# Kernel tuning notes

Measured on AMD Instinct MI355X. Metric: run time of the kernel, lower is better.

The kernel has to match this reference:

```python
import jax, jax.numpy as jnp
import numpy as np
from jax import lax

C = 128; G = 8; K = 3; P = K * K; GC = C // G
N, H, W = 4, 96, 96
EPS = 1e-5

def conv_bn_silu(x, w, gamma, beta, rmean, rvar, stride, pad):
    # Conv2d(bias=False) + BatchNorm2d(eval) + SiLU, NCHW
    y = lax.conv_general_dilated(x, w, (stride, stride), [(pad, pad), (pad, pad)],
                                 dimension_numbers=('NCHW', 'OIHW', 'NCHW'))
    s = gamma / jnp.sqrt(rvar + EPS)
    y = y * s[None, :, None, None] + (beta - rmean * s)[None, :, None, None]
    return y * jax.nn.sigmoid(y)

def dcnv3(x, dw_w, dw_b, ln_g, ln_b, off_w, off_b, m_w, m_b, ip_w, ip_b, op_w, op_b):
    # InternImage DCNv3, channels-last input (N,H,W,C), k=3 s=1 pad=1 dil=1 group=G, offset_scale=1
    n, h, w, c = x.shape
    xp = x @ ip_w.T + ip_b  # input_proj
    # offset/mask branch: depthwise 3x3 conv + LayerNorm + GELU on the ORIGINAL input
    dw = lax.conv_general_dilated(x, dw_w, (1, 1), [(1, 1), (1, 1)],
                                  dimension_numbers=('NHWC', 'HWIO', 'NHWC'),
                                  feature_group_count=c) + dw_b
    dw = (dw - dw.mean(-1, keepdims=True)) / jnp.sqrt(dw.var(-1, keepdims=True) + EPS) * ln_g + ln_b
    dw = jax.nn.gelu(dw)
    off = (dw @ off_w.T + off_b).reshape(n, h, w, G, P, 2)  # (..., (dx, dy))
    m = jax.nn.softmax((dw @ m_w.T + m_b).reshape(n, h, w, G, P), -1)
    pad = 1
    hp, wp = h + 2 * pad, w + 2 * pad
    xpad = jnp.pad(xp, ((0, 0), (pad, pad), (pad, pad), (0, 0))).reshape(n, hp, wp, G, GC)
    ky, kx = jnp.meshgrid(jnp.arange(-1, 2, dtype=x.dtype), jnp.arange(-1, 2, dtype=x.dtype), indexing='ij')
    # absolute sampling coords in padded image (grid_sample align_corners=False equivalent)
    py = (jnp.arange(h, dtype=x.dtype) + pad)[None, :, None, None, None] + ky.reshape(-1) + off[..., 1]
    px = (jnp.arange(w, dtype=x.dtype) + pad)[None, None, :, None, None] + kx.reshape(-1) + off[..., 0]
    yf = jnp.floor(py); xf = jnp.floor(px)
    wy = py - yf; wx = px - xf
    y0 = yf.astype(jnp.int32); x0 = xf.astype(jnp.int32)
    n_idx = jnp.arange(n)[:, None, None, None, None]
    g_idx = jnp.arange(G)[None, None, None, :, None]

    def gat(yi, xi):
        valid = ((yi >= 0) & (yi < hp) & (xi >= 0) & (xi < wp)).astype(x.dtype)
        v = xpad[n_idx, jnp.clip(yi, 0, hp - 1), jnp.clip(xi, 0, wp - 1), g_idx]  # (n,h,w,G,P,GC)
        return v * valid[..., None]

    v = (gat(y0, x0) * ((1 - wy) * (1 - wx))[..., None]
         + gat(y0, x0 + 1) * ((1 - wy) * wx)[..., None]
         + gat(y0 + 1, x0) * (wy * (1 - wx))[..., None]
         + gat(y0 + 1, x0 + 1) * (wy * wx)[..., None])
    out = jnp.einsum('nhwgpc,nhwgp->nhwgc', v, m).reshape(n, h, w, c)
    return out @ op_w.T + op_b  # output_proj

def _forward(x0, x1, x2, conv_w, conv_g, conv_b, conv_rm, conv_rv,
             conv1_w, conv1_g, conv1_b, conv1_rm, conv1_rv,
             conv2_w, conv2_g, conv2_b, conv2_rm, conv2_rv,
             dw_w, dw_b, ln_g, ln_b, off_w, off_b, m_w, m_b, ip_w, ip_b, op_w, op_b):
    n, _, h, w = x0.shape
    # x1: 256 ch > 128 -> self.conv (1x1); smaller spatial -> bilinear upsample to HW
    y1 = conv_bn_silu(x1, conv_w, conv_g, conv_b, conv_rm, conv_rv, 1, 0)
    feat_up1 = jax.image.resize(y1, (n, C, h, w), method='bilinear')
    # x2: 64 ch < 128 -> self.conv1 (1x1); larger spatial -> self.conv2 (3x3 s2) to HW
    y2 = conv_bn_silu(x2, conv1_w, conv1_g, conv1_b, conv1_rm, conv1_rv, 1, 0)
    feat_up2 = conv_bn_silu(y2, conv2_w, conv2_g, conv2_b, conv2_rm, conv2_rv, 2, 1)
    d1 = dcnv3(feat_up1.transpose(0, 2, 3, 1), dw_w, dw_b, ln_g, ln_b, off_w, off_b, m_w, m_b, ip_w, ip_b, op_w, op_b)
    d2 = dcnv3(feat_up2.transpose(0, 2, 3, 1), dw_w, dw_b, ln_g, ln_b, off_w, off_b, m_w, m_b, ip_w, ip_b, op_w, op_b)
    a1 = jax.nn.relu(d1).transpose(0, 3, 1, 2)
    a2 = jax.nn.relu(d2).transpose(0, 3, 1, 2)
    return jnp.concatenate([a1, x0, a2], axis=1)  # (N, 3C, H, W)

def setup_inputs():
    ks = jax.random.split(jax.random.key(0), 24)
    f = jnp.float32
    return {
        'x0': jax.random.normal(ks[0], (N, C, H, W), f),
        'x1': jax.random.normal(ks[1], (N, 2 * C, H // 2, W // 2), f),
        'x2': jax.random.normal(ks[2], (N, C // 2, 2 * H, 2 * W), f),
        'conv_w': jax.random.normal(ks[3], (C, 2 * C, 1, 1), f) * 0.05,
        'conv_g': jnp.ones((C,), f), 'conv_b': jnp.zeros((C,), f),
        'conv_rm': jax.random.normal(ks[4], (C,), f) * 0.1,
        'conv_rv': jax.random.uniform(ks[5], (C,), f) + 0.5,
        'conv1_w': jax.random.normal(ks[6], (C, C // 2, 1, 1), f) * 0.08,
        'conv1_g': jnp.ones((C,), f), 'conv1_b': jnp.zeros((C,), f),
        'conv1_rm': jax.random.normal(ks[7], (C,), f) * 0.1,
        'conv1_rv': jax.random.uniform(ks[8], (C,), f) + 0.5,
        'conv2_w': jax.random.normal(ks[9], (C, C, 3, 3), f) * 0.03,
        'conv2_g': jnp.ones((C,), f), 'conv2_b': jnp.zeros((C,), f),
        'conv2_rm': jax.random.normal(ks[10], (C,), f) * 0.1,
        'conv2_rv': jax.random.uniform(ks[11], (C,), f) + 0.5,
        'dw_w': jax.random.normal(ks[12], (3, 3, 1, C), f) * 0.1,
        'dw_b': jnp.zeros((C,), f),
        'ln_g': jnp.ones((C,), f), 'ln_b': jnp.zeros((C,), f),
        'off_w': jax.random.normal(ks[13], (G * P * 2, C), f) * 0.01,
        'off_b': jnp.zeros((G * P * 2,), f),
        'm_w': jax.random.normal(ks[14], (G * P, C), f) * 0.05,
        'm_b': jnp.zeros((G * P,), f),
        'ip_w': jax.random.normal(ks[15], (C, C), f) * 0.05,
        'ip_b': jnp.zeros((C,), f),
        'op_w': jax.random.normal(ks[16], (C, C), f) * 0.05,
        'op_b': jnp.zeros((C,), f),
    }

def reference(x0, x1, x2, conv_w, conv_g, conv_b, conv_rm, conv_rv,
              conv1_w, conv1_g, conv1_b, conv1_rm, conv1_rv,
              conv2_w, conv2_g, conv2_b, conv2_rm, conv2_rv,
              dw_w, dw_b, ln_g, ln_b, off_w, off_b, m_w, m_b, ip_w, ip_b, op_w, op_b):
    return _forward(x0, x1, x2, conv_w, conv_g, conv_b, conv_rm, conv_rv,
                    conv1_w, conv1_g, conv1_b, conv1_rm, conv1_rv,
                    conv2_w, conv2_g, conv2_b, conv2_rm, conv2_rv,
                    dw_w, dw_b, ln_g, ln_b, off_w, off_b, m_w, m_b, ip_w, ip_b, op_w, op_b)
```

## Files before the change

kernel.cpp:

```cpp
#include <hip/hip_runtime.h>
#include <cstdint>
#include <cstddef>

#define EPSV 1e-5f
#define NPIX 9216
#define LDA 136
#define LDK 72

typedef __bf16 bf16;
typedef _Float16 f16;
typedef __attribute__((ext_vector_type(8))) __bf16 bf16x8;
typedef __attribute__((ext_vector_type(4))) __bf16 bf16x4;
typedef __attribute__((ext_vector_type(2))) _Float16 f16x2;
typedef __attribute__((ext_vector_type(4))) float  f32x4;

__device__ __forceinline__ float silu_f(float v) { return v / (1.f + __expf(-v)); }

__global__ __launch_bounds__(256) void prep_kernel(
    const float* __restrict__ conv_w, const float* __restrict__ conv_g,
    const float* __restrict__ conv_b, const float* __restrict__ conv_rm, const float* __restrict__ conv_rv,
    const float* __restrict__ conv1_w, const float* __restrict__ conv1_g,
    const float* __restrict__ conv1_b, const float* __restrict__ conv1_rm, const float* __restrict__ conv1_rv,
    const float* __restrict__ conv2_w, const float* __restrict__ conv2_g,
    const float* __restrict__ conv2_bb, const float* __restrict__ conv2_rm, const float* __restrict__ conv2_rv,
    const float* __restrict__ ip_w, const float* __restrict__ op_w,
    const float* __restrict__ off_w, const float* __restrict__ m_w,
    const float* __restrict__ off_b, const float* __restrict__ m_b,
    float* __restrict__ WTSf, bf16* __restrict__ WTSb)
{
  int idx = blockIdx.x * 256 + threadIdx.x;
  if (idx < 608) {
    if (idx < 128) {
      int co = idx;
      float s = conv_g[co] * rsqrtf(conv_rv[co] + EPSV);
      WTSf[idx] = conv_b[co] - conv_rm[co] * s;
    } else if (idx < 256) {
      int co = idx - 128;
      float s = conv1_g[co] * rsqrtf(conv1_rv[co] + EPSV);
      WTSf[idx] = conv1_b[co] - conv1_rm[co] * s;
    } else if (idx < 384) {
      int co = idx - 256;
      float s = conv2_g[co] * rsqrtf(conv2_rv[co] + EPSV);
      WTSf[idx] = conv2_bb[co] - conv2_rm[co] * s;
    } else {
      int col = idx - 384;
      WTSf[idx] = (col < 144) ? off_b[col] : (col < 216 ? m_b[col - 144] : 0.f);
    }
  } else {
    int j = idx - 608;
    if (j < 32768) {
      int co = j >> 8, ci = j & 255;
      float s = conv_g[co] * rsqrtf(conv_rv[co] + EPSV);
      WTSb[j] = (bf16)(conv_w[co * 256 + ci] * s);
    } else if (j < 40960) {
      int r = j - 32768; int co = r >> 6, ci = r & 63;
      float s = conv1_g[co] * rsqrtf(conv1_rv[co] + EPSV);
      WTSb[j] = (bf16)(conv1_w[co * 64 + ci] * s);
    } else if (j < 188416) {
      int r = j - 40960; int kp = r >> 14; int rr = r & 16383;
      int co = rr >> 7, ci = rr & 127;
      float s = conv2_g[co] * rsqrtf(conv2_rv[co] + EPSV);
      WTSb[j] = (bf16)(conv2_w[(co * 128 + ci) * 9 + kp] * s);
    } else if (j < 204800) {
      int r = j - 188416; int co = r >> 7, ci = r & 127;
      WTSb[j] = (bf16)ip_w[co * 128 + ci];
    } else if (j < 233472) {
      int r = j - 204800; int co = r >> 7, ci = r & 127;
      float v = (co < 144) ? off_w[co * 128 + ci] : (co < 216 ? m_w[(co - 144) * 128 + ci] : 0.f);
      WTSb[j] = (bf16)v;
    } else if (j < 249856) {
      int r = j - 233472; int co = r >> 7, ci = r & 127;
      WTSb[j] = (bf16)op_w[co * 128 + ci];
    }
  }
}

__global__ __launch_bounds__(256) void c1x1_mfma_kernel(
    const float* __restrict__ x, const bf16* __restrict__ W,
    const float* __restrict__ bias, int K, int HW, bf16* __restrict__ outb)
{
  __shared__ bf16 As[64 * LDK];
  __shared__ bf16 Bs[128 * LDK];
  int m0 = blockIdx.x << 6;
  int t = threadIdx.x;
  int n = m0 / HW; int hw0 = m0 - n * HW;
  const float* xn = x + (size_t)n * K * HW;
  int wv = t >> 6, lane = t & 63;
  int lrow = lane & 15, q = lane >> 4;
  int n0 = wv * 32;
  f32x4 acc[4][2];
#pragma unroll
  for (int i = 0; i < 4; ++i)
#pragma unroll
    for (int j = 0; j < 2; ++j)
#pragma unroll
      for (int e = 0; e < 4; ++e) acc[i][j][e] = 0.f;

  for (int k0 = 0; k0 < K; k0 += 64) {
    if (k0) __syncthreads();
    for (int i = t; i < 1024; i += 256) {
      int px = i & 63; int ci4 = (i >> 6) << 2;
      bf16x4 p;
#pragma unroll
      for (int j = 0; j < 4; ++j)
        p[j] = (bf16)xn[(size_t)(k0 + ci4 + j) * HW + hw0 + px];
      *(bf16x4*)&As[px * LDK + ci4] = p;
    }
    for (int i = t; i < 1024; i += 256) {
      int co = i >> 3; int k8 = (i & 7) << 3;
      *(bf16x8*)&Bs[co * LDK + k8] = *(const bf16x8*)&W[(size_t)co * K + k0 + k8];
    }
    __syncthreads();
#pragma unroll
    for (int ks = 0; ks < 2; ++ks) {
      int ko = ks * 32 + q * 8;
      bf16x8 bfr0 = *(const bf16x8*)&Bs[(n0 + lrow) * LDK + ko];
      bf16x8 bfr1 = *(const bf16x8*)&Bs[(n0 + 16 + lrow) * LDK + ko];
#pragma unroll
      for (int mi = 0; mi < 4; ++mi) {
        bf16x8 afr = *(const bf16x8*)&As[(mi * 16 + lrow) * LDK + ko];
        acc[mi][0] = __builtin_amdgcn_mfma_f32_16x16x32_bf16(afr, bfr0, acc[mi][0], 0, 0, 0);
        acc[mi][1] = __builtin_amdgcn_mfma_f32_16x16x32_bf16(afr, bfr1, acc[mi][1], 0, 0, 0);
      }
    }
  }
#pragma unroll
  for (int mi = 0; mi < 4; ++mi) {
#pragma unroll
    for (int nj = 0; nj < 2; ++nj) {
      int co = n0 + nj * 16 + lrow;
      float bb = bias[co];
#pragma unroll
      for (int r = 0; r < 4; ++r) {
        int m = m0 + mi * 16 + q * 4 + r;
        outb[(size_t)m * 128 + co] = (bf16)silu_f(acc[mi][nj][r] + bb);
      }
    }
  }
}

__global__ __launch_bounds__(256) void upsample_kernel(
    const bf16* __restrict__ y1b, bf16* __restrict__ feat1b)
{
  int idx = blockIdx.x * 256 + threadIdx.x;
  int c4 = (idx & 31) << 2;
  int pw = idx >> 5;
  int ow = pw % 96; int t1 = pw / 96;
  int oh = t1 % 96; int n = t1 / 96;
  float sh = oh * 0.5f - 0.25f, sw = ow * 0.5f - 0.25f;
  float hf = floorf(sh), wf = floorf(sw);
  float fy = sh - hf, fx = sw - wf;
  int h0 = (int)hf, w0 = (int)wf;
  int h0c = max(h0, 0), h1c = min(h0 + 1, 47);
  int w0c = max(w0, 0), w1c = min(w0 + 1, 47);
  const bf16* yn = y1b + (size_t)n * 2304 * 128 + c4;
  bf16x4 v00 = *(const bf16x4*)&yn[(h0c * 48 + w0c) * 128];
  bf16x4 v01 = *(const bf16x4*)&yn[(h0c * 48 + w1c) * 128];
  bf16x4 v10 = *(const bf16x4*)&yn[(h1c * 48 + w0c) * 128];
  bf16x4 v11 = *(const bf16x4*)&yn[(h1c * 48 + w1c) * 128];
  bf16x4 o;
#pragma unroll
  for (int e = 0; e < 4; ++e) {
    float v = (1.f - fy) * ((1.f - fx) * (float)v00[e] + fx * (float)v01[e])
            + fy * ((1.f - fx) * (float)v10[e] + fx * (float)v11[e]);
    o[e] = (bf16)v;
  }
  *(bf16x4*)&feat1b[((size_t)n * NPIX + oh * 96 + ow) * 128 + c4] = o;
}

__global__ __launch_bounds__(256) void conv2_mfma_kernel(
    const bf16* __restrict__ y2b, const bf16* __restrict__ W2b,
    const float* __restrict__ b2, bf16* __restrict__ feat2b)
{
  __shared__ bf16 As[64 * LDA];
  __shared__ bf16 Bs[128 * LDA];
  int m0 = blockIdx.x << 6;
  int t = threadIdx.x;
  int wv = t >> 6, lane = t & 63;
  int lrow = lane & 15, q = lane >> 4;
  int n0 = wv * 32;
  f32x4 acc[4][2];
#pragma unroll
  for (int i = 0; i < 4; ++i)
#pragma unroll
    for (int j = 0; j < 2; ++j)
#pragma unroll
      for (int e = 0; e < 4; ++e) acc[i][j][e] = 0.f;
  bf16x8 zv;
#pragma unroll
  for (int e = 0; e < 8; ++e) zv[e] = (bf16)0.f;

  for (int kp = 0; kp < 9; ++kp) {
    int kh = kp / 3, kw = kp - kh * 3;
    __syncthreads();
    for (int i = t; i < 1024; i += 256) {
      int row = i >> 4; int c8 = (i & 15) << 3;
      int m = m0 + row;
      int nimg = m / NPIX; int hw = m - nimg * NPIX;
      int oh = hw / 96, ow = hw - oh * 96;
      int ih = 2 * oh - 1 + kh, iw = 2 * ow - 1 + kw;
      bf16x8 v = zv;
      if ((unsigned)ih < 192u && (unsigned)iw < 192u)
        v = *(const bf16x8*)&y2b[(((size_t)nimg * 192 + ih) * 192 + iw) * 128 + c8];
      *(bf16x8*)&As[row * LDA + c8] = v;
    }
    const bf16* Wk = W2b + kp * 16384;
    for (int i = t; i < 2048; i += 256) {
      int nn = i >> 4; int k8 = (i & 15) << 3;
      *(bf16x8*)&Bs[nn * LDA + k8] = *(const bf16x8*)&Wk[nn * 128 + k8];
    }
    __syncthreads();
#pragma unroll
    for (int ks = 0; ks < 4; ++ks) {
      bf16x8 bfr0 = *(const bf16x8*)&Bs[(n0 + lrow) * LDA + ks * 32 + q * 8];
      bf16x8 bfr1 = *(const bf16x8*)&Bs[(n0 + 16 + lrow) * LDA + ks * 32 + q * 8];
#pragma unroll
      for (int mi = 0; mi < 4; ++mi) {
        bf16x8 afr = *(const bf16x8*)&As[(mi * 16 + lrow) * LDA + ks * 32 + q * 8];
        acc[mi][0] = __builtin_amdgcn_mfma_f32_16x16x32_bf16(afr, bfr0, acc[mi][0], 0, 0, 0);
        acc[mi][1] = __builtin_amdgcn_mfma_f32_16x16x32_bf16(afr, bfr1, acc[mi][1], 0, 0, 0);
      }
    }
  }
#pragma unroll
  for (int mi = 0; mi < 4; ++mi) {
#pragma unroll
    for (int nj = 0; nj < 2; ++nj) {
      int co = n0 + nj * 16 + lrow;
      float bb = b2[co];
#pragma unroll
      for (int r = 0; r < 4; ++r) {
        int m = m0 + mi * 16 + q * 4 + r;
        feat2b[(size_t)m * 128 + co] = (bf16)silu_f(acc[mi][nj][r] + bb);
      }
    }
  }
}

__global__ __launch_bounds__(256) void mm_bf16_kernel(
    const bf16* __restrict__ A, const bf16* __restrict__ W,
    const float* __restrict__ bias, int Nc, int ostride, int act,
    int store_mode, void* __restrict__ outp)
{
  __shared__ bf16 As[64 * LDA];
  __shared__ bf16 Bs[128 * LDA];
  int m0 = blockIdx.x << 6;
  int nb = blockIdx.y << 7;
  int cols_here = Nc - nb; if (cols_here > 128) cols_here = 128;
  int t = threadIdx.x;
  for (int i = t; i < 1024; i += 256) {
    int row = i >> 4; int c8 = (i & 15) << 3;
    *(bf16x8*)&As[row * LDA + c8] = *(const bf16x8*)&A[(size_t)(m0 + row) * 128 + c8];
  }
  bf16x8 zv;
#pragma unroll
  for (int e = 0; e < 8; ++e) zv[e] = (bf16)0.f;
  for (int i = t; i < 2048; i += 256) {
    int n = i >> 4; int k8 = (i & 15) << 3;
    bf16x8 v = (n < cols_here) ? *(const bf16x8*)&W[(size_t)(nb + n) * 128 + k8] : zv;
    *(bf16x8*)&Bs[n * LDA + k8] = v;
  }
  __syncthreads();

  int wv = t >> 6, lane = t & 63;
  int lrow = lane & 15, q = lane >> 4;
  int n0 = wv * 32;
  f32x4 acc[4][2];
#pragma unroll
  for (int i = 0; i < 4; ++i)
#pragma unroll
    for (int j = 0; j < 2; ++j)
#pragma unroll
      for (int e = 0; e < 4; ++e) acc[i][j][e] = 0.f;

#pragma unroll
  for (int ks = 0; ks < 4; ++ks) {
    bf16x8 bfr0 = *(const bf16x8*)&Bs[(n0 + lrow) * LDA + ks * 32 + q * 8];
    bf16x8 bfr1 = *(const bf16x8*)&Bs[(n0 + 16 + lrow) * LDA + ks * 32 + q * 8];
#pragma unroll
    for (int mi = 0; mi < 4; ++mi) {
      bf16x8 afr = *(const bf16x8*)&As[(mi * 16 + lrow) * LDA + ks * 32 + q * 8];
      acc[mi][0] = __builtin_amdgcn_mfma_f32_16x16x32_bf16(afr, bfr0, acc[mi][0], 0, 0, 0);
      acc[mi][1] = __builtin_amdgcn_mfma_f32_16x16x32_bf16(afr, bfr1, acc[mi][1], 0, 0, 0);
    }
  }

  float* outf = (float*)outp;
  bf16*  outb = (bf16*)outp;
  f16*   outh = (f16*)outp;
#pragma unroll
  for (int mi = 0; mi < 4; ++mi) {
#pragma unroll
    for (int nj = 0; nj < 2; ++nj) {
      int col = nb + n0 + nj * 16 + lrow;
      if (col >= Nc) continue;
      float bb = bias[col];
#pragma unroll
      for (int r = 0; r < 4; ++r) {
        int m = m0 + mi * 16 + q * 4 + r;
        float v = acc[mi][nj][r] + bb;
        if (act == 1) v = fmaxf(v, 0.f);
        if (store_mode == 0) {
          outf[(size_t)m * ostride + col] = v;
        } else if (store_mode == 2) {
          outb[(size_t)m * 128 + col] = (bf16)v;
        } else if (store_mode == 3) {
          outh[(size_t)m * ostride + col] = (f16)v;
        } else {
          int nn = m / NPIX; int hw = m - nn * NPIX;
          int img = nn & 3; int choff = (nn >= 4) ? 256 : 0;
          outf[((size_t)(img * 384 + choff + col)) * NPIX + hw] = v;
        }
      }
    }
  }
}

__global__ __launch_bounds__(256) void dwln_kernel(
    const bf16* __restrict__ featb, const float* __restrict__ dw_w,
    const float* __restrict__ dw_b, const float* __restrict__ ln_g,
    const float* __restrict__ ln_b, bf16* __restrict__ dwgb)
{
  __shared__ float Wts[1152];
  __shared__ float Pb[384];
  int t = threadIdx.x;
  for (int i = t; i < 1152; i += 256) Wts[i] = dw_w[i];
  for (int i = t; i < 384; i += 256)
    Pb[i] = (i < 128) ? dw_b[i] : (i < 256 ? ln_g[i - 128] : ln_b[i - 256]);
  __syncthreads();

  int pxl = t >> 4;
  int c8 = (t & 15) << 3;
  int bid = blockIdx.x;
  int wg = (bid & 7) * 576 + (bid >> 3);
  int pixel = wg * 16 + pxl;
  int n = pixel / NPIX; int hw = pixel - n * NPIX;
  int h = hw / 96; int w = hw - h * 96;
  const bf16* fn = featb + (size_t)n * NPIX * 128 + c8;
  bf16x8 zv;
#pragma unroll
  for (int e = 0; e < 8; ++e) zv[e] = (bf16)0.f;

  bf16x8 v[9];
#pragma unroll
  for (int p = 0; p < 9; ++p) {
    int hh = h + p / 3 - 1, ww = w + (p % 3) - 1;
    bool valid = ((unsigned)hh < 96u) && ((unsigned)ww < 96u);
    int hc = min(max(hh, 0), 95), wc = min(max(ww, 0), 95);
    bf16x8 x = *(const bf16x8*)&fn[(hc * 96 + wc) * 128];
    v[p] = valid ? x : zv;
  }

  float acc[8];
#pragma unroll
  for (int e = 0; e < 8; ++e) acc[e] = Pb[c8 + e];
#pragma unroll
  for (int p = 0; p < 9; ++p) {
    f32x4 w0 = *(const f32x4*)&Wts[p * 128 + c8];
    f32x4 w1 = *(const f32x4*)&Wts[p * 128 + c8 + 4];
#pragma unroll
    for (int e = 0; e < 4; ++e) {
      acc[e]     += (float)v[p][e]     * w0[e];
      acc[4 + e] += (float)v[p][4 + e] * w1[e];
    }
  }

  float s = 0.f, qs = 0.f;
#pragma unroll
  for (int e = 0; e < 8; ++e) { s += acc[e]; qs += acc[e] * acc[e]; }
#pragma unroll
  for (int off = 8; off > 0; off >>= 1) {
    s  += __shfl_xor(s, off);
    qs += __shfl_xor(qs, off);
  }
  float mean = s * (1.f / 128.f);
  float var = qs * (1.f / 128.f) - mean * mean;
  float rstd = rsqrtf(var + EPSV);
  bf16x8 o;
#pragma unroll
  for (int e = 0; e < 8; ++e) {
    float xn = (acc[e] - mean) * rstd * Pb[128 + c8 + e] + Pb[256 + c8 + e];
    float z = 0.7978845608028654f * (xn + 0.044715f * xn * xn * xn);
    float th;
    if (z > 15.f) th = 1.f;
    else if (z < -15.f) th = -1.f;
    else { float e2 = __expf(2.f * z); th = (e2 - 1.f) / (e2 + 1.f); }
    o[e] = (bf16)(0.5f * xn * (1.f + th));
  }
  *(bf16x8*)&dwgb[(size_t)pixel * 128 + c8] = o;
}

__global__ __launch_bounds__(256, 6) void sample_kernel(
    const bf16* __restrict__ xpb, const f16* __restrict__ offm,
    const bf16* __restrict__ Wop, const float* __restrict__ op_b,
    float* __restrict__ out)
{
  __shared__ uint32_t Sd[16 * 112];
  __shared__ float Pm[16 * 72];
  __shared__ bf16 Avs[16 * LDA];
  const f16* S = (const f16*)Sd;
  int t = threadIdx.x;
  int bid = blockIdx.x;
  int wg = (bid & 7) * 576 + (bid >> 3);
  {
    const uint32_t* src = (const uint32_t*)(offm + (size_t)wg * 16 * 224);
    for (int i = t; i < 1792; i += 256) Sd[i] = src[i];
  }
  __syncthreads();
  if (t < 128) {
    int px = t >> 3, gg = t & 7;
    const f16* L = S + px * 224 + 144 + gg * 9;
    float l[9]; float mx = -1e30f;
#pragma unroll
    for (int p = 0; p < 9; ++p) { l[p] = (float)L[p]; mx = fmaxf(mx, l[p]); }
    float se = 0.f;
#pragma unroll
    for (int p = 0; p < 9; ++p) { l[p] = __expf(l[p] - mx); se += l[p]; }
    float inv = 1.f / se;
    float* Pp = Pm + px * 72 + gg * 9;
#pragma unroll
    for (int p = 0; p < 9; ++p) Pp[p] = l[p] * inv;
  }
  __syncthreads();
  int pxl = t >> 4;
  int tid16 = t & 15;
  int g = tid16 >> 1;
  int c8 = (tid16 & 1) << 3;
  int pixel = wg * 16 + pxl;
  int n = pixel / NPIX; int hw = pixel - n * NPIX;
  int h = hw / 96; int w = hw - h * 96;
  const f16* Sp = S + pxl * 224 + g * 18;
  const float* Pp = Pm + pxl * 72 + g * 9;
  const bf16* xpn = xpb + (size_t)n * NPIX * 128 + g * 16 + c8;
  float acc[8];
#pragma unroll
  for (int e = 0; e < 8; ++e) acc[e] = 0.f;
#pragma unroll 1
  for (int kh = 0; kh < 3; ++kh) {
#pragma unroll
    for (int kw = 0; kw < 3; ++kw) {
      int p = kh * 3 + kw;
      f16x2 d2 = *(const f16x2*)&Sp[p * 2];
      float dx = (float)d2.x, dy = (float)d2.y;
      float pyu = (float)(h + kh - 1) + dy;
      float pxu = (float)(w + kw - 1) + dx;
      float yf = floorf(pyu), xf = floorf(pxu);
      float wy = pyu - yf, wx = pxu - xf;
      int y0 = (int)yf, x0 = (int)xf;
      float ay0 = ((unsigned)y0 < 96u) ? (1.f - wy) : 0.f;
      float ay1 = ((unsigned)(y0 + 1) < 96u) ? wy : 0.f;
      float ax0 = ((unsigned)x0 < 96u) ? (1.f - wx) : 0.f;
      float ax1 = ((unsigned)(x0 + 1) < 96u) ? wx : 0.f;
      int y0c = min(max(y0, 0), 95), y1c = min(max(y0 + 1, 0), 95);
      int x0c = min(max(x0, 0), 95), x1c = min(max(x0 + 1, 0), 95);
      float mp = Pp[p];
      float w00 = ay0 * ax0 * mp, w01 = ay0 * ax1 * mp;
      float w10 = ay1 * ax0 * mp, w11 = ay1 * ax1 * mp;
      bf16x8 v00 = *(const bf16x8*)&xpn[(y0c * 96 + x0c) * 128];
      bf16x8 v01 = *(const bf16x8*)&xpn[(y0c * 96 + x1c) * 128];
      bf16x8 v10 = *(const bf16x8*)&xpn[(y1c * 96 + x0c) * 128];
      bf16x8 v11 = *(const bf16x8*)&xpn[(y1c * 96 + x1c) * 128];
#pragma unroll
      for (int e = 0; e < 8; ++e) {
        acc[e] += w00 * (float)v00[e] + w01 * (float)v01[e]
                + w10 * (float)v10[e] + w11 * (float)v11[e];
      }
    }
  }
  bf16x8 o;
#pragma unroll
  for (int e = 0; e < 8; ++e) o[e] = (bf16)acc[e];
  *(bf16x8*)&Avs[pxl * LDA + g * 16 + c8] = o;
  __syncthreads();

  {
    int wv = t >> 6, lane = t & 63;
    int lrow = lane & 15, q = lane >> 4;
    int n0 = wv * 32;
    f32x4 pacc[2];
#pragma unroll
    for (int j = 0; j < 2; ++j)
#pragma unroll
      for (int e = 0; e < 4; ++e) pacc[j][e] = 0.f;
#pragma unroll
    for (int ks = 0; ks < 4; ++ks) {
      int ko = ks * 32 + q * 8;
      bf16x8 afr  = *(const bf16x8*)&Avs[lrow * LDA + ko];
      bf16x8 bfr0 = *(const bf16x8*)&Wop[(size_t)(n0 + lrow) * 128 + ko];
      bf16x8 bfr1 = *(const bf16x8*)&Wop[(size_t)(n0 + 16 + lrow) * 128 + ko];
      pacc[0] = __builtin_amdgcn_mfma_f32_16x16x32_bf16(afr, bfr0, pacc[0], 0, 0, 0);
      pacc[1] = __builtin_amdgcn_mfma_f32_16x16x32_bf16(afr, bfr1, pacc[1], 0, 0, 0);
    }
    int nn = (wg * 16) / NPIX;
    int hwb = wg * 16 - nn * NPIX;
    int img = nn & 3; int choff = (nn >= 4) ? 256 : 0;
#pragma unroll
    for (int nj = 0; nj < 2; ++nj) {
      int col = n0 + nj * 16 + lrow;
      float bb = op_b[col];
      float* oc = out + ((size_t)(img * 384 + choff + col)) * NPIX + hwb;
#pragma unroll
      for (int r = 0; r < 4; ++r) {
        int px = q * 4 + r;
        oc[px] = fmaxf(pacc[nj][r] + bb, 0.f);
      }
    }
  }
}

__global__ __launch_bounds__(256) void copy_x0_kernel(
    const float4* __restrict__ x0, float4* __restrict__ out)
{
  int idx = blockIdx.x * 256 + threadIdx.x;
  int n = idx / (128 * 2304);
  int r = idx - n * (128 * 2304);
  out[(size_t)(n * 384 + 128) * 2304 + r] = x0[(size_t)n * 128 * 2304 + r];
}

extern "C" void kernel_launch(void* const* d_in, const int* in_sizes, int n_in,
                              void* d_out, int out_size, void* d_ws, size_t ws_size,
                              hipStream_t stream)
{
  (void)in_sizes; (void)n_in; (void)out_size; (void)ws_size;
  const float* x0      = (const float*)d_in[0];
  const float* x1      = (const float*)d_in[1];
  const float* x2      = (const float*)d_in[2];
  const float* conv_w  = (const float*)d_in[3];
  const float* conv_g  = (const float*)d_in[4];
  const float* conv_b  = (const float*)d_in[5];
  const float* conv_rm = (const float*)d_in[6];
  const float* conv_rv = (const float*)d_in[7];
  const float* conv1_w = (const float*)d_in[8];
  const float* conv1_g = (const float*)d_in[9];
  const float* conv1_b = (const float*)d_in[10];
  const float* conv1_rm= (const float*)d_in[11];
  const float* conv1_rv= (const float*)d_in[12];
  const float* conv2_w = (const float*)d_in[13];
  const float* conv2_g = (const float*)d_in[14];
  const float* conv2_b = (const float*)d_in[15];
  const float* conv2_rm= (const float*)d_in[16];
  const float* conv2_rv= (const float*)d_in[17];
  const float* dw_w    = (const float*)d_in[18];
  const float* dw_b    = (const float*)d_in[19];
  const float* ln_g    = (const float*)d_in[20];
  const float* ln_b    = (const float*)d_in[21];
  const float* off_w   = (const float*)d_in[22];
  const float* off_b   = (const float*)d_in[23];
  const float* m_w     = (const float*)d_in[24];
  const float* m_b     = (const float*)d_in[25];
  const float* ip_w    = (const float*)d_in[26];
  const float* ip_b    = (const float*)d_in[27];
  const float* op_w    = (const float*)d_in[28];
  const float* op_b    = (const float*)d_in[29];
  float* out = (float*)d_out;
  char* WS = (char*)d_ws;

  bf16* featb  = (bf16*)WS;
  bf16* feat1b = featb;
  bf16* feat2b = featb + 4718592;
  bf16* y2b    = (bf16*)(WS + 18874368);
  bf16* xpb    = (bf16*)(WS + 18874368);
  bf16* dwgb   = (bf16*)(WS + 37748736);
  bf16* y1b    = (bf16*)(WS + 56623104);
  f16*  offm   = (f16*)(WS + 58982400);
  float* WTSf  = (float*)(WS + 125042688);
  bf16*  WTSb  = (bf16*)(WS + 125045120);

  float* b1f  = WTSf;
  float* b1bf = WTSf + 128;
  float* b2f  = WTSf + 256;
  float* bomf = WTSf + 384;
  bf16* W1b  = WTSb;
  bf16* W1bb = WTSb + 32768;
  bf16* W2b  = WTSb + 40960;
  bf16* Wipb = WTSb + 188416;
  bf16* Womb = WTSb + 204800;
  bf16* Wopb = WTSb + 233472;

  prep_kernel<<<979, 256, 0, stream>>>(
      conv_w, conv_g, conv_b, conv_rm, conv_rv,
      conv1_w, conv1_g, conv1_b, conv1_rm, conv1_rv,
      conv2_w, conv2_g, conv2_b, conv2_rm, conv2_rv,
      ip_w, op_w, off_w, m_w, off_b, m_b, WTSf, WTSb);

  c1x1_mfma_kernel<<<144, 256, 0, stream>>>(x1, W1b, b1f, 256, 2304, y1b);
  upsample_kernel<<<4608, 256, 0, stream>>>(y1b, feat1b);

  c1x1_mfma_kernel<<<2304, 256, 0, stream>>>(x2, W1bb, b1bf, 64, 36864, y2b);
  conv2_mfma_kernel<<<576, 256, 0, stream>>>(y2b, W2b, b2f, feat2b);

  mm_bf16_kernel<<<dim3(1152, 1), 256, 0, stream>>>(featb, Wipb, ip_b, 128, 128, 0, 2, xpb);
  dwln_kernel<<<4608, 256, 0, stream>>>(featb, dw_w, dw_b, ln_g, ln_b, dwgb);
  mm_bf16_kernel<<<dim3(1152, 2), 256, 0, stream>>>(dwgb, Womb, bomf, 224, 224, 0, 3, offm);
  sample_kernel<<<4608, 256, 0, stream>>>(xpb, offm, Wopb, op_b, out);

  copy_x0_kernel<<<4608, 256, 0, stream>>>((const float4*)x0, (float4*)out);
}
```

Baseline: 384.0 us.

## Double sample-kernel pixel tile and stage output projection through LDS for coalesced stores

Each sample_kernel block now handles 32 pixels with 512 threads instead of 16 pixels with 256. The output-projection waves are split across row halves and column quarters. Results go into an LDS buffer that reuses the offset and mask storage, then are written to the NCHW output as float4 rows of 32 contiguous pixels per channel, replacing scattered 4-byte stores. The trade-offs are an extra barrier, more LDS per block, a launch bound of 6 blocks of 512 threads that may tighten register limits, and 16-byte LDS reads at a 33-float row stride whose alignment is not guaranteed.

```diff
diff --git a/kernel.cpp b/kernel.cpp
--- a/kernel.cpp
+++ b/kernel.cpp
@@ -390,24 +390,26 @@
   *(bf16x8*)&dwgb[(size_t)pixel * 128 + c8] = o;
 }
 
-__global__ __launch_bounds__(256, 6) void sample_kernel(
+__global__ __launch_bounds__(512, 6) void sample_kernel(
     const bf16* __restrict__ xpb, const f16* __restrict__ offm,
     const bf16* __restrict__ Wop, const float* __restrict__ op_b,
     float* __restrict__ out)
 {
-  __shared__ uint32_t Sd[16 * 112];
-  __shared__ float Pm[16 * 72];
-  __shared__ bf16 Avs[16 * LDA];
+  __shared__ char LB[32256];
+  uint32_t* Sd = (uint32_t*)LB;
+  float*    Pm = (float*)(LB + 14336);
+  bf16*     Avs = (bf16*)(LB + 23552);
+  float*    Cs = (float*)LB;
   const f16* S = (const f16*)Sd;
   int t = threadIdx.x;
   int bid = blockIdx.x;
-  int wg = (bid & 7) * 576 + (bid >> 3);
+  int wg = (bid & 7) * 288 + (bid >> 3);
   {
-    const uint32_t* src = (const uint32_t*)(offm + (size_t)wg * 16 * 224);
-    for (int i = t; i < 1792; i += 256) Sd[i] = src[i];
+    const uint32_t* src = (const uint32_t*)(offm + (size_t)wg * 32 * 224);
+    for (int i = t; i < 3584; i += 512) Sd[i] = src[i];
   }
   __syncthreads();
-  if (t < 128) {
+  if (t < 256) {
     int px = t >> 3, gg = t & 7;
     const f16* L = S + px * 224 + 144 + gg * 9;
     float l[9]; float mx = -1e30f;
@@ -422,61 +424,64 @@
     for (int p = 0; p < 9; ++p) Pp[p] = l[p] * inv;
   }
   __syncthreads();
-  int pxl = t >> 4;
-  int tid16 = t & 15;
-  int g = tid16 >> 1;
-  int c8 = (tid16 & 1) << 3;
-  int pixel = wg * 16 + pxl;
-  int n = pixel / NPIX; int hw = pixel - n * NPIX;
-  int h = hw / 96; int w = hw - h * 96;
-  const f16* Sp = S + pxl * 224 + g * 18;
-  const float* Pp = Pm + pxl * 72 + g * 9;
-  const bf16* xpn = xpb + (size_t)n * NPIX * 128 + g * 16 + c8;
-  float acc[8];
-#pragma unroll
-  for (int e = 0; e < 8; ++e) acc[e] = 0.f;
+  {
+    int pxl = t >> 4;
+    int tid16 = t & 15;
+    int g = tid16 >> 1;
+    int c8 = (tid16 & 1) << 3;
+    int pixel = wg * 32 + pxl;
+    int n = pixel / NPIX; int hw = pixel - n * NPIX;
+    int h = hw / 96; int w = hw - h * 96;
+    const f16* Sp = S + pxl * 224 + g * 18;
+    const float* Pp = Pm + pxl * 72 + g * 9;
+    const bf16* xpn = xpb + (size_t)n * NPIX * 128 + g * 16 + c8;
+    float acc[8];
+#pragma unroll
+    for (int e = 0; e < 8; ++e) acc[e] = 0.f;
 #pragma unroll 1
-  for (int kh = 0; kh < 3; ++kh) {
-#pragma unroll
-    for (int kw = 0; kw < 3; ++kw) {
-      int p = kh * 3 + kw;
-      f16x2 d2 = *(const f16x2*)&Sp[p * 2];
-      float dx = (float)d2.x, dy = (float)d2.y;
-      float pyu = (float)(h + kh - 1) + dy;
-      float pxu = (float)(w + kw - 1) + dx;
-      float yf = floorf(pyu), xf = floorf(pxu);
-      float wy = pyu - yf, wx = pxu - xf;
-      int y0 = (int)yf, x0 = (int)xf;
-      float ay0 = ((unsigned)y0 < 96u) ? (1.f - wy) : 0.f;
-      float ay1 = ((unsigned)(y0 + 1) < 96u) ? wy : 0.f;
-      float ax0 = ((unsigned)x0 < 96u) ? (1.f - wx) : 0.f;
-      float ax1 = ((unsigned)(x0 + 1) < 96u) ? wx : 0.f;
-      int y0c = min(max(y0, 0), 95), y1c = min(max(y0 + 1, 0), 95);
-      int x0c = min(max(x0, 0), 95), x1c = min(max(x0 + 1, 0), 95);
-      float mp = Pp[p];
-      float w00 = ay0 * ax0 * mp, w01 = ay0 * ax1 * mp;
-      float w10 = ay1 * ax0 * mp, w11 = ay1 * ax1 * mp;
-      bf16x8 v00 = *(const bf16x8*)&xpn[(y0c * 96 + x0c) * 128];
-      bf16x8 v01 = *(const bf16x8*)&xpn[(y0c * 96 + x1c) * 128];
-      bf16x8 v10 = *(const bf16x8*)&xpn[(y1c * 96 + x0c) * 128];
-      bf16x8 v11 = *(const bf16x8*)&xpn[(y1c * 96 + x1c) * 128];
-#pragma unroll
-      for (int e = 0; e < 8; ++e) {
-        acc[e] += w00 * (float)v00[e] + w01 * (float)v01[e]
-                + w10 * (float)v10[e] + w11 * (float)v11[e];
+    for (int kh = 0; kh < 3; ++kh) {
+#pragma unroll
+      for (int kw = 0; kw < 3; ++kw) {
+        int p = kh * 3 + kw;
+        f16x2 d2 = *(const f16x2*)&Sp[p * 2];
+        float dx = (float)d2.x, dy = (float)d2.y;
+        float pyu = (float)(h + kh - 1) + dy;
+        float pxu = (float)(w + kw - 1) + dx;
+        float yf = floorf(pyu), xf = floorf(pxu);
+        float wy = pyu - yf, wx = pxu - xf;
+        int y0 = (int)yf, x0 = (int)xf;
+        float ay0 = ((unsigned)y0 < 96u) ? (1.f - wy) : 0.f;
+        float ay1 = ((unsigned)(y0 + 1) < 96u) ? wy : 0.f;
+        float ax0 = ((unsigned)x0 < 96u) ? (1.f - wx) : 0.f;
+        float ax1 = ((unsigned)(x0 + 1) < 96u) ? wx : 0.f;
+        int y0c = min(max(y0, 0), 95), y1c = min(max(y0 + 1, 0), 95);
+        int x0c = min(max(x0, 0), 95), x1c = min(max(x0 + 1, 0), 95);
+        float mp = Pp[p];
+        float w00 = ay0 * ax0 * mp, w01 = ay0 * ax1 * mp;
+        float w10 = ay1 * ax0 * mp, w11 = ay1 * ax1 * mp;
+        bf16x8 v00 = *(const bf16x8*)&xpn[(y0c * 96 + x0c) * 128];
+        bf16x8 v01 = *(const bf16x8*)&xpn[(y0c * 96 + x1c) * 128];
+        bf16x8 v10 = *(const bf16x8*)&xpn[(y1c * 96 + x0c) * 128];
+        bf16x8 v11 = *(const bf16x8*)&xpn[(y1c * 96 + x1c) * 128];
+#pragma unroll
+        for (int e = 0; e < 8; ++e) {
+          acc[e] += w00 * (float)v00[e] + w01 * (float)v01[e]
+                  + w10 * (float)v10[e] + w11 * (float)v11[e];
+        }
       }
     }
-  }
-  bf16x8 o;
-#pragma unroll
-  for (int e = 0; e < 8; ++e) o[e] = (bf16)acc[e];
-  *(bf16x8*)&Avs[pxl * LDA + g * 16 + c8] = o;
+    bf16x8 o;
+#pragma unroll
+    for (int e = 0; e < 8; ++e) o[e] = (bf16)acc[e];
+    *(bf16x8*)&Avs[pxl * LDA + g * 16 + c8] = o;
+  }
   __syncthreads();
 
   {
     int wv = t >> 6, lane = t & 63;
     int lrow = lane & 15, q = lane >> 4;
-    int n0 = wv * 32;
+    int mrow0 = (wv & 1) * 16;
+    int n0 = (wv >> 1) * 32;
     f32x4 pacc[2];
 #pragma unroll
     for (int j = 0; j < 2; ++j)
@@ -485,25 +490,35 @@
 #pragma unroll
     for (int ks = 0; ks < 4; ++ks) {
       int ko = ks * 32 + q * 8;
-      bf16x8 afr  = *(const bf16x8*)&Avs[lrow * LDA + ko];
+      bf16x8 afr  = *(const bf16x8*)&Avs[(mrow0 + lrow) * LDA + ko];
       bf16x8 bfr0 = *(const bf16x8*)&Wop[(size_t)(n0 + lrow) * 128 + ko];
       bf16x8 bfr1 = *(const bf16x8*)&Wop[(size_t)(n0 + 16 + lrow) * 128 + ko];
       pacc[0] = __builtin_amdgcn_mfma_f32_16x16x32_bf16(afr, bfr0, pacc[0], 0, 0, 0);
       pacc[1] = __builtin_amdgcn_mfma_f32_16x16x32_bf16(afr, bfr1, pacc[1], 0, 0, 0);
     }
-    int nn = (wg * 16) / NPIX;
-    int hwb = wg * 16 - nn * NPIX;
-    int img = nn & 3; int choff = (nn >= 4) ? 256 : 0;
 #pragma unroll
     for (int nj = 0; nj < 2; ++nj) {
       int col = n0 + nj * 16 + lrow;
       float bb = op_b[col];
-      float* oc = out + ((size_t)(img * 384 + choff + col)) * NPIX + hwb;
 #pragma unroll
       for (int r = 0; r < 4; ++r) {
-        int px = q * 4 + r;
-        oc[px] = fmaxf(pacc[nj][r] + bb, 0.f);
+        int px = mrow0 + q * 4 + r;
+        Cs[col * 33 + px] = fmaxf(pacc[nj][r] + bb, 0.f);
       }
+    }
+  }
+  __syncthreads();
+
+  {
+    int nn = (wg * 32) / NPIX;
+    int hwb = wg * 32 - nn * NPIX;
+    int img = nn & 3; int choff = (nn >= 4) ? 256 : 0;
+    float* ob = out + (size_t)(img * 384 + choff) * NPIX + hwb;
+#pragma unroll
+    for (int i = t; i < 1024; i += 512) {
+      int col = i >> 3, f4 = i & 7;
+      f32x4 v = *(const f32x4*)&Cs[col * 33 + f4 * 4];
+      *(f32x4*)&ob[(size_t)col * NPIX + f4 * 4] = v;
     }
   }
 }
@@ -592,7 +607,7 @@
   mm_bf16_kernel<<<dim3(1152, 1), 256, 0, stream>>>(featb, Wipb, ip_b, 128, 128, 0, 2, xpb);
   dwln_kernel<<<4608, 256, 0, stream>>>(featb, dw_w, dw_b, ln_g, ln_b, dwgb);
   mm_bf16_kernel<<<dim3(1152, 2), 256, 0, stream>>>(dwgb, Womb, bomf, 224, 224, 0, 3, offm);
-  sample_kernel<<<4608, 256, 0, stream>>>(xpb, offm, Wopb, op_b, out);
+  sample_kernel<<<2304, 512, 0, stream>>>(xpb, offm, Wopb, op_b, out);
 
   copy_x0_kernel<<<4608, 256, 0, stream>>>((const float4*)x0, (float4*)out);
 }
```

New measurement: 374.4 us. 1.03x faster.
